# Performance work log

Measured on AMD Instinct MI355X. Metric: run time of the kernel, lower is better.

The kernel has to match this reference:

```python
import jax, jax.numpy as jnp
import numpy as np


def setup_inputs() -> dict:
    key = jax.random.key(0)
    X = jax.random.normal(key, (8, 64, 64, 64), dtype=jnp.float32)
    return {"X": X}


def reference(X):
    N, C, h, w = X.shape
    x1 = X.reshape(N, C, h * w)            # [N, C, HW]
    x2 = jnp.transpose(x1, (0, 2, 1))      # [N, HW, C]
    scores = jnp.einsum('bnc,bcm->bnm', x2, x1)  # [N, HW, HW]
    c = jax.nn.softmax(scores, axis=2)
    out = jnp.einsum('bnm,bmc->bnc', c, x2)      # [N, HW, C]
    out = jnp.transpose(out, (0, 2, 1)).reshape(N, C, h, w)
    return out
```

## Files before the change

kernel.cpp:

```cpp
#include <hip/hip_runtime.h>
#include <math.h>


#define SEQ 4096
#define DIM 64
#define LDB 72
#define LDO 68
#define LDS2 68
#define QSCALE 1.2011224087864498f

typedef __attribute__((ext_vector_type(8))) short  short8;
typedef __attribute__((ext_vector_type(4))) float  f32x4;

__device__ __forceinline__ unsigned short f2bf(float f) {
    union { float f; unsigned int u; } x; x.f = f;
    unsigned int u = x.u + 0x7FFFu + ((x.u >> 16) & 1u);
    return (unsigned short)(u >> 16);
}
__device__ __forceinline__ float bf2f(unsigned short h) {
    union { unsigned int u; float f; } x; x.u = ((unsigned int)h) << 16; return x.f;
}
__device__ __forceinline__ float fast_exp2(float x) {
#if __has_builtin(__builtin_amdgcn_exp2f)
    return __builtin_amdgcn_exp2f(x);
#else
    float r;
    asm("v_exp_f32 %0, %1\n\ts_nop 0" : "=v"(r) : "v"(x));
    return r;
#endif
}
__device__ __forceinline__ float fast_rcp(float x) {
#if __has_builtin(__builtin_amdgcn_rcpf)
    return __builtin_amdgcn_rcpf(x);
#else
    return 1.f / x;
#endif
}

__global__ __launch_bounds__(256) void prepass4(const float* __restrict__ X,
                                                unsigned short* __restrict__ Kf,
                                                unsigned short* __restrict__ Vf,
                                                float* __restrict__ Norms,
                                                float* __restrict__ MaxPart) {
    __shared__ __align__(16) unsigned short sT[64 * LDS2];
    __shared__ __align__(16) unsigned short sVu[64 * LDS2];
    __shared__ float sRed[4];
    const int b = blockIdx.y, m0 = blockIdx.x * 64;
    const float* Xb = X + (size_t)b * DIM * SEQ;
    const int t = threadIdx.x, w = t >> 6;
    const int mw = t & 15, cg = t >> 4;

    #pragma unroll
    for (int cr = 0; cr < 4; ++cr) {
        const int c = cg * 4 + cr;
        const f32x4 v = *(const f32x4*)(Xb + (size_t)c * SEQ + m0 + 4 * mw);
        *(ushort4*)(sVu + c * LDS2 + 4 * mw) =
            make_ushort4(f2bf(v.x), f2bf(v.y), f2bf(v.z), f2bf(v.w));
        sT[(4 * mw + 0) * LDS2 + c] = f2bf(v.x * QSCALE);
        sT[(4 * mw + 1) * LDS2 + c] = f2bf(v.y * QSCALE);
        sT[(4 * mw + 2) * LDS2 + c] = f2bf(v.z * QSCALE);
        sT[(4 * mw + 3) * LDS2 + c] = f2bf(v.w * QSCALE);
    }
    __syncthreads();
    const int m = t >> 2, ck = t & 3;

    const short8 a0 = *(const short8*)(sT + m * LDS2 + ck * 16);
    const short8 a1 = *(const short8*)(sT + m * LDS2 + ck * 16 + 8);
    {
        const size_t base = (size_t)b * 262144 + (size_t)(m0 >> 5) * 2048;
        #pragma unroll
        for (int j = 0; j < 2; ++j) {
            const int chunk = 2 * ck + j;
            const int tile = m >> 5, mt = (m >> 4) & 1;
            const int quad = chunk & 3, ks = chunk >> 2;
            const size_t off = base + (size_t)(tile * 4 + mt * 2 + ks) * 512
                                    + (size_t)(quad * 16 + (m & 15)) * 8;
            *(short8*)(Kf + off) = j ? a1 : a0;
        }
    }
    float s = 0.f;
    #pragma unroll
    for (int i = 0; i < 8; ++i) {
        const float f0 = bf2f((unsigned short)a0[i]);
        const float f1 = bf2f((unsigned short)a1[i]);
        s += f0 * f0 + f1 * f1;
    }
    s += __shfl_xor(s, 1);
    s += __shfl_xor(s, 2);
    const float nm = sqrtf(s);
    if (ck == 0) Norms[(size_t)b * SEQ + m0 + m] = nm;

    {
        const int ctv = (t >> 6) & 3, lv = t & 63;
        const int qv = lv >> 4, l15v = lv & 15;
        const int cidx = (16 * ctv + l15v) * LDS2;
        const size_t vbase = (size_t)b * 262144 + (size_t)(m0 >> 5) * 2048
                           + (size_t)ctv * 512 + (size_t)lv * 8;
        #pragma unroll
        for (int tl = 0; tl < 2; ++tl) {
            const ushort4 g0 = *(const ushort4*)(sVu + cidx + tl * 32 + 4 * qv);
            const ushort4 g1 = *(const ushort4*)(sVu + cidx + tl * 32 + 16 + 4 * qv);
            union { ushort4 g[2]; short8 v; } cat;
            cat.g[0] = g0; cat.g[1] = g1;
            *(short8*)(Vf + vbase + (size_t)tl * 2048) = cat.v;
        }
    }

    float mx = nm;
    #pragma unroll
    for (int d = 4; d < 64; d <<= 1) mx = fmaxf(mx, __shfl_xor(mx, d));
    if ((t & 63) == 0) sRed[w] = mx;
    __syncthreads();
    if (t == 0)
        MaxPart[b * 64 + blockIdx.x] =
            fmaxf(fmaxf(sRed[0], sRed[1]), fmaxf(sRed[2], sRed[3]));
}

#define LOADK(DST)                                                                 \
    {                                                                              \
        _Pragma("unroll")                                                          \
        for (int mt_ = 0; mt_ < 2; ++mt_) {                                        \
            _Pragma("unroll")                                                      \
            for (int ks_ = 0; ks_ < 2; ++ks_)                                      \
                DST[mt_][ks_] = *(const short8*)(kp + (mt_ * 2 + ks_) * 512);      \
        }                                                                          \
    }

#define LOADV(DST)                                                                 \
    {                                                                              \
        _Pragma("unroll")                                                          \
        for (int ct_ = 0; ct_ < 4; ++ct_)                                          \
            DST[ct_] = *(const short8*)(vp + ct_ * 512);                           \
    }

#define ATTN_STEP(KF, VF)                                                          \
    {                                                                              \
        f32x4 a_[2][2];                                                            \
        __builtin_amdgcn_s_setprio(1);                                             \
        _Pragma("unroll")                                                          \
        for (int qt_ = 0; qt_ < 2; ++qt_) {                                        \
            _Pragma("unroll")                                                      \
            for (int mt_ = 0; mt_ < 2; ++mt_) {                                    \
                f32x4 s_ = cin[qt_];                                               \
                s_ = __builtin_amdgcn_mfma_f32_16x16x32_bf16(KF[mt_][0], qf[qt_][0], s_, 0, 0, 0); \
                s_ = __builtin_amdgcn_mfma_f32_16x16x32_bf16(KF[mt_][1], qf[qt_][1], s_, 0, 0, 0); \
                a_[qt_][mt_] = s_;                                                 \
            }                                                                      \
        }                                                                          \
        __builtin_amdgcn_s_setprio(0);                                             \
        short8 pa_[2];                                                             \
        _Pragma("unroll")                                                          \
        for (int qt_ = 0; qt_ < 2; ++qt_) {                                        \
            union { unsigned u[4]; short8 v; } pk_;                                \
            _Pragma("unroll")                                                      \
            for (int mt_ = 0; mt_ < 2; ++mt_) {                                    \
                const float p0_ = fast_exp2(a_[qt_][mt_][0]);                      \
                const float p1_ = fast_exp2(a_[qt_][mt_][1]);                      \
                const float p2_ = fast_exp2(a_[qt_][mt_][2]);                      \
                const float p3_ = fast_exp2(a_[qt_][mt_][3]);                      \
                lp4[qt_] += (f32x4){p0_, p1_, p2_, p3_};                           \
                pk_.u[2 * mt_ + 0] = __builtin_amdgcn_perm(__float_as_uint(p1_), __float_as_uint(p0_), 0x07060302u); \
                pk_.u[2 * mt_ + 1] = __builtin_amdgcn_perm(__float_as_uint(p3_), __float_as_uint(p2_), 0x07060302u); \
            }                                                                      \
            pa_[qt_] = pk_.v;                                                      \
        }                                                                          \
        __builtin_amdgcn_s_setprio(1);                                             \
        _Pragma("unroll")                                                          \
        for (int qt_ = 0; qt_ < 2; ++qt_) {                                        \
            _Pragma("unroll")                                                      \
            for (int ct_ = 0; ct_ < 4; ++ct_)                                      \
                acc_o[qt_][ct_] = __builtin_amdgcn_mfma_f32_16x16x32_bf16(pa_[qt_], VF[ct_], acc_o[qt_][ct_], 0, 0, 0); \
        }                                                                          \
        __builtin_amdgcn_s_setprio(0);                                             \
    }

template <bool PARTIAL>
__global__ __launch_bounds__(128) void attn_split4(const unsigned short* __restrict__ Kf,
                                                   const unsigned short* __restrict__ Vf,
                                                   const float* __restrict__ Norms,
                                                   const float* __restrict__ MaxPart,
                                                   unsigned short* __restrict__ Obf,
                                                   float* __restrict__ Lbase,
                                                   float* __restrict__ Out,
                                                   int niter) {
    __shared__ __align__(16) float sO[64 * LDO];

    const int tid  = threadIdx.x;
    const int lane = tid & 63;
    const int w    = tid >> 6;
    const int l15  = lane & 15;
    const int quad = lane >> 4;

    const int b   = blockIdx.y;
    const int s0  = blockIdx.x * 64;
    const int h   = blockIdx.z;
    const int kt0 = h * niter;
    const unsigned short* Kfb = Kf + (size_t)b * 262144;
    const unsigned short* Vfb = Vf + (size_t)b * 262144;

    float mxn = MaxPart[b * 64 + lane];
    #pragma unroll
    for (int d = 1; d < 64; d <<= 1) mxn = fmaxf(mxn, __shfl_xor(mxn, d));

    short8 qf[2][2];
    f32x4 cin[2];
    const int qtile = (s0 + 32 * w) >> 5;
    #pragma unroll
    for (int qt = 0; qt < 2; ++qt) {
        #pragma unroll
        for (int ks = 0; ks < 2; ++ks)
            qf[qt][ks] = *(const short8*)(Kfb + (size_t)(qtile * 4 + qt * 2 + ks) * 512 + lane * 8);
        const float mrow = Norms[(size_t)b * SEQ + s0 + 32 * w + 16 * qt + l15] * mxn;
        cin[qt] = (f32x4){-mrow, -mrow, -mrow, -mrow};
    }

    f32x4 acc_o[2][4];
    #pragma unroll
    for (int qt = 0; qt < 2; ++qt)
        #pragma unroll
        for (int ct = 0; ct < 4; ++ct) acc_o[qt][ct] = (f32x4){0.f, 0.f, 0.f, 0.f};
    f32x4 lp4[2];
    lp4[0] = (f32x4){0.f, 0.f, 0.f, 0.f};
    lp4[1] = (f32x4){0.f, 0.f, 0.f, 0.f};

    const unsigned short* kp = Kfb + (size_t)kt0 * 2048 + lane * 8;
    const unsigned short* vp = Vfb + (size_t)kt0 * 2048 + lane * 8;

    short8 kA[2][2], kB[2][2];
    LOADK(kA);
    kp += 2048;

    for (int it = 0; it < niter; it += 2) {
        short8 vfA[4];
        LOADV(vfA); vp += 2048;
        LOADK(kB);  kp += 2048;
        ATTN_STEP(kA, vfA);

        short8 vfB[4];
        LOADV(vfB); vp += 2048;
        LOADK(kA);  kp += 2048;
        ATTN_STEP(kB, vfB);
    }

    float lp[2];
    #pragma unroll
    for (int qt = 0; qt < 2; ++qt) {
        lp[qt] = (lp4[qt][0] + lp4[qt][1]) + (lp4[qt][2] + lp4[qt][3]);
        lp[qt] += __shfl_xor(lp[qt], 16);
        lp[qt] += __shfl_xor(lp[qt], 32);
    }

    if (PARTIAL) {
        if (quad == 0) {
            #pragma unroll
            for (int qt = 0; qt < 2; ++qt)
                (Lbase + (size_t)h * 8 * SEQ)[(size_t)b * SEQ + s0 + 32 * w + 16 * qt + l15] = lp[qt];
        }
    } else {
        #pragma unroll
        for (int qt = 0; qt < 2; ++qt) {
            float inv[4];
            #pragma unroll
            for (int r = 0; r < 4; ++r) inv[r] = fast_rcp(__shfl(lp[qt], 4 * quad + r));
            #pragma unroll
            for (int ct = 0; ct < 4; ++ct)
                #pragma unroll
                for (int r = 0; r < 4; ++r) acc_o[qt][ct][r] *= inv[r];
        }
    }

    #pragma unroll
    for (int qt = 0; qt < 2; ++qt)
        #pragma unroll
        for (int ct = 0; ct < 4; ++ct) {
            const int c = 16 * ct + l15;
            #pragma unroll
            for (int r = 0; r < 4; ++r)
                sO[c * LDO + 32 * w + 16 * qt + 4 * quad + r] = acc_o[qt][ct][r];
        }
    __syncthreads();
    const int mw = tid & 15, cg = tid >> 4;
    if (PARTIAL) {
        unsigned short* Op = Obf + (size_t)h * 8 * DIM * SEQ;
        #pragma unroll
        for (int cc = 0; cc < 8; ++cc) {
            const int c = cg + 8 * cc;
            const f32x4 v = *(const f32x4*)(sO + c * LDO + 4 * mw);
            *(ushort4*)(Op + ((size_t)b * DIM + c) * SEQ + s0 + 4 * mw) =
                make_ushort4(f2bf(v.x), f2bf(v.y), f2bf(v.z), f2bf(v.w));
        }
    } else {
        #pragma unroll
        for (int cc = 0; cc < 8; ++cc) {
            const int c = cg + 8 * cc;
            const f32x4 v = *(const f32x4*)(sO + c * LDO + 4 * mw);
            *(f32x4*)(Out + ((size_t)b * DIM + c) * SEQ + s0 + 4 * mw) = v;
        }
    }
}

__global__ __launch_bounds__(256) void combine4(const unsigned short* __restrict__ Obf,
                                                const float* __restrict__ Lp,
                                                float* __restrict__ Out) {
    const int gid = blockIdx.x * 256 + threadIdx.x;
    const size_t base = (size_t)gid * 4;
    const int s = (int)(base & 4095);
    const int b = (int)(base >> 18);
    f32x4 os = (f32x4){0.f, 0.f, 0.f, 0.f};
    f32x4 ls = (f32x4){0.f, 0.f, 0.f, 0.f};
    #pragma unroll
    for (int h = 0; h < 4; ++h) {
        const ushort4 o = *(const ushort4*)(Obf + (size_t)h * 2097152 + base);
        os[0] += bf2f(o.x); os[1] += bf2f(o.y); os[2] += bf2f(o.z); os[3] += bf2f(o.w);
        const f32x4 l = *(const f32x4*)(Lp + (size_t)h * 8 * SEQ + b * SEQ + s);
        #pragma unroll
        for (int i = 0; i < 4; ++i) ls[i] += l[i];
    }
    f32x4 o;
    #pragma unroll
    for (int i = 0; i < 4; ++i) o[i] = os[i] / ls[i];
    *(f32x4*)(Out + base) = o;
}

__global__ __launch_bounds__(256, 2) void attn_fallback(const float* __restrict__ X,
                                                        float* __restrict__ Out) {
    __shared__ __align__(16) unsigned char smem[27648];
    unsigned short* sK = (unsigned short*)smem;
    unsigned short* sV = (unsigned short*)(smem + 9216);
    unsigned short* sP = (unsigned short*)(smem + 18432);
    float*          sO = (float*)smem;
    const int tid  = threadIdx.x;
    const int lane = tid & 63;
    const int w    = tid >> 6;
    const int l15  = lane & 15;
    const int quad = lane >> 4;
    const int b  = blockIdx.y;
    const int s0 = blockIdx.x * 64;
    const float* Xb = X + (size_t)b * DIM * SEQ;
    const int mgrp = tid & 15;
    const int c0   = tid >> 4;

    for (int cc = 0; cc < 4; ++cc) {
        int c = c0 + 16 * cc;
        const f32x4 v = *(const f32x4*)(Xb + (size_t)c * SEQ + s0 + 4 * mgrp);
        sK[(4 * mgrp + 0) * LDB + c] = f2bf(v.x);
        sK[(4 * mgrp + 1) * LDB + c] = f2bf(v.y);
        sK[(4 * mgrp + 2) * LDB + c] = f2bf(v.z);
        sK[(4 * mgrp + 3) * LDB + c] = f2bf(v.w);
    }
    __syncthreads();
    short8 qf0, qf1;
    {
        const int row = 16 * w + l15;
        qf0 = *(const short8*)(sK + row * LDB + quad * 8);
        qf1 = *(const short8*)(sK + row * LDB + 32 + quad * 8);
    }
    __syncthreads();
    f32x4 acc_o[4];
    for (int ct = 0; ct < 4; ++ct) acc_o[ct] = (f32x4){0.f, 0.f, 0.f, 0.f};
    float m_i[4] = {-1e30f, -1e30f, -1e30f, -1e30f};
    float l_i[4] = {0.f, 0.f, 0.f, 0.f};
    for (int kt = 0; kt < SEQ / 64; ++kt) {
        const int m0 = kt * 64;
        for (int cc = 0; cc < 4; ++cc) {
            int c = c0 + 16 * cc;
            const f32x4 v = *(const f32x4*)(Xb + (size_t)c * SEQ + m0 + 4 * mgrp);
            unsigned short h0 = f2bf(v.x), h1 = f2bf(v.y), h2 = f2bf(v.z), h3 = f2bf(v.w);
            *(ushort4*)(sV + c * LDB + 4 * mgrp) = make_ushort4(h0, h1, h2, h3);
            sK[(4 * mgrp + 0) * LDB + c] = h0;
            sK[(4 * mgrp + 1) * LDB + c] = h1;
            sK[(4 * mgrp + 2) * LDB + c] = h2;
            sK[(4 * mgrp + 3) * LDB + c] = h3;
        }
        __syncthreads();
        short8 vf[2][4];
        for (int ks = 0; ks < 2; ++ks)
            for (int ct = 0; ct < 4; ++ct)
                vf[ks][ct] = *(const short8*)(sV + (16 * ct + l15) * LDB + ks * 32 + quad * 8);
        f32x4 acc_s[4];
        for (int mt = 0; mt < 4; ++mt) {
            const int row = 16 * mt + l15;
            const short8 kf0 = *(const short8*)(sK + row * LDB + quad * 8);
            const short8 kf1 = *(const short8*)(sK + row * LDB + 32 + quad * 8);
            f32x4 a = (f32x4){0.f, 0.f, 0.f, 0.f};
            a = __builtin_amdgcn_mfma_f32_16x16x32_bf16(qf0, kf0, a, 0, 0, 0);
            a = __builtin_amdgcn_mfma_f32_16x16x32_bf16(qf1, kf1, a, 0, 0, 0);
            acc_s[mt] = a;
        }
        float alpha[4];
        for (int r = 0; r < 4; ++r) {
            float mx = fmaxf(fmaxf(acc_s[0][r], acc_s[1][r]), fmaxf(acc_s[2][r], acc_s[3][r]));
            mx = fmaxf(mx, __shfl_xor(mx, 1));
            mx = fmaxf(mx, __shfl_xor(mx, 2));
            mx = fmaxf(mx, __shfl_xor(mx, 4));
            mx = fmaxf(mx, __shfl_xor(mx, 8));
            const float mnew = fmaxf(m_i[r], mx);
            alpha[r] = __expf(m_i[r] - mnew);
            m_i[r] = mnew;
        }
        float rowsum[4] = {0.f, 0.f, 0.f, 0.f};
        unsigned short pb[4][4];
        for (int mt = 0; mt < 4; ++mt)
            for (int r = 0; r < 4; ++r) {
                const float p = __expf(acc_s[mt][r] - m_i[r]);
                rowsum[r] += p;
                pb[mt][r] = f2bf(p);
            }
        for (int r = 0; r < 4; ++r) {
            float s = rowsum[r];
            s += __shfl_xor(s, 1);
            s += __shfl_xor(s, 2);
            s += __shfl_xor(s, 4);
            s += __shfl_xor(s, 8);
            l_i[r] = alpha[r] * l_i[r] + s;
        }
        for (int ct = 0; ct < 4; ++ct)
            for (int r = 0; r < 4; ++r)
                acc_o[ct][r] *= alpha[r];
        for (int mt = 0; mt < 4; ++mt)
            for (int r = 0; r < 4; ++r)
                sP[(16 * w + quad * 4 + r) * LDB + l15 + 16 * mt] = pb[mt][r];
        __syncthreads();
        const short8 pf0 = *(const short8*)(sP + (16 * w + l15) * LDB + quad * 8);
        const short8 pf1 = *(const short8*)(sP + (16 * w + l15) * LDB + 32 + quad * 8);
        for (int ct = 0; ct < 4; ++ct) {
            acc_o[ct] = __builtin_amdgcn_mfma_f32_16x16x32_bf16(pf0, vf[0][ct], acc_o[ct], 0, 0, 0);
            acc_o[ct] = __builtin_amdgcn_mfma_f32_16x16x32_bf16(pf1, vf[1][ct], acc_o[ct], 0, 0, 0);
        }
    }
    float inv[4];
    for (int r = 0; r < 4; ++r) inv[r] = 1.f / l_i[r];
    for (int ct = 0; ct < 4; ++ct) {
        const int c = 16 * ct + l15;
        for (int r = 0; r < 4; ++r)
            sO[c * LDO + 16 * w + quad * 4 + r] = acc_o[ct][r] * inv[r];
    }
    __syncthreads();
    for (int cc = 0; cc < 4; ++cc) {
        const int c = c0 + 16 * cc;
        const f32x4 v = *(const f32x4*)(sO + c * LDO + 4 * mgrp);
        *(f32x4*)(Out + (size_t)b * DIM * SEQ + (size_t)c * SEQ + s0 + 4 * mgrp) = v;
    }
}

extern "C" void kernel_launch(void* const* d_in, const int* in_sizes, int n_in,
                              void* d_out, int out_size, void* d_ws, size_t ws_size,
                              hipStream_t stream) {
    const float* X = (const float*)d_in[0];
    float* Out = (float*)d_out;
    const size_t elems = (size_t)8 * SEQ * DIM;
    const size_t offVf    = elems * 2;
    const size_t offNorms = offVf + elems * 2;
    const size_t offMaxP  = offNorms + (size_t)8 * SEQ * 4;
    const size_t offObf   = offMaxP + 8 * 64 * 4;
    const size_t offLp    = offObf + 4 * elems * 2;
    const size_t need     = offLp + 4 * (size_t)8 * SEQ * 4;

    if (ws_size >= need) {
        unsigned short* Kf = (unsigned short*)d_ws;
        unsigned short* Vf = (unsigned short*)((char*)d_ws + offVf);
        float* Norms   = (float*)((char*)d_ws + offNorms);
        float* MaxPart = (float*)((char*)d_ws + offMaxP);
        unsigned short* Obf = (unsigned short*)((char*)d_ws + offObf);
        float* Lp = (float*)((char*)d_ws + offLp);
        prepass4<<<dim3(64, 8), 256, 0, stream>>>(X, Kf, Vf, Norms, MaxPart);
        attn_split4<true><<<dim3(64, 8, 4), 128, 0, stream>>>(Kf, Vf, Norms, MaxPart,
                                                              Obf, Lp, nullptr, 32);
        combine4<<<(int)(elems / 1024), 256, 0, stream>>>(Obf, Lp, Out);
    } else {
        attn_fallback<<<dim3(64, 8), 256, 0, stream>>>(X, Out);
    }
}
```

Before: 118.5 us.

## Double query rows per wave in split attention to reuse K/V fragments

Each wave now handles 64 query rows (four 16-row tiles) instead of 32. Every K/V fragment loaded from memory therefore feeds twice as many MFMAs, and the grid is halved to 32x8x4 blocks. Block indices are remapped so batch is the fastest-varying dimension, the s_setprio hints are dropped, and the LDS output staging uses a new odd row stride. The cost is higher register use (more accumulators and Q fragments), fewer blocks to fill the GPU, and 16-byte LDS reads on a stride of 133 floats that may not be 16-byte aligned.

```diff
diff --git a/kernel.cpp b/kernel.cpp
--- a/kernel.cpp
+++ b/kernel.cpp
@@ -6,6 +6,7 @@
 #define DIM 64
 #define LDB 72
 #define LDO 68
+#define LDO2 133
 #define LDS2 68
 #define QSCALE 1.2011224087864498f
 
@@ -135,10 +136,9 @@
 
 #define ATTN_STEP(KF, VF)                                                          \
     {                                                                              \
-        f32x4 a_[2][2];                                                            \
-        __builtin_amdgcn_s_setprio(1);                                             \
+        f32x4 a_[4][2];                                                            \
         _Pragma("unroll")                                                          \
-        for (int qt_ = 0; qt_ < 2; ++qt_) {                                        \
+        for (int qt_ = 0; qt_ < 4; ++qt_) {                                        \
             _Pragma("unroll")                                                      \
             for (int mt_ = 0; mt_ < 2; ++mt_) {                                    \
                 f32x4 s_ = cin[qt_];                                               \
@@ -147,10 +147,9 @@
                 a_[qt_][mt_] = s_;                                                 \
             }                                                                      \
         }                                                                          \
-        __builtin_amdgcn_s_setprio(0);                                             \
-        short8 pa_[2];                                                             \
+        short8 pa_[4];                                                             \
         _Pragma("unroll")                                                          \
-        for (int qt_ = 0; qt_ < 2; ++qt_) {                                        \
+        for (int qt_ = 0; qt_ < 4; ++qt_) {                                        \
             union { unsigned u[4]; short8 v; } pk_;                                \
             _Pragma("unroll")                                                      \
             for (int mt_ = 0; mt_ < 2; ++mt_) {                                    \
@@ -164,26 +163,24 @@
             }                                                                      \
             pa_[qt_] = pk_.v;                                                      \
         }                                                                          \
-        __builtin_amdgcn_s_setprio(1);                                             \
         _Pragma("unroll")                                                          \
-        for (int qt_ = 0; qt_ < 2; ++qt_) {                                        \
+        for (int qt_ = 0; qt_ < 4; ++qt_) {                                        \
             _Pragma("unroll")                                                      \
             for (int ct_ = 0; ct_ < 4; ++ct_)                                      \
                 acc_o[qt_][ct_] = __builtin_amdgcn_mfma_f32_16x16x32_bf16(pa_[qt_], VF[ct_], acc_o[qt_][ct_], 0, 0, 0); \
         }                                                                          \
-        __builtin_amdgcn_s_setprio(0);                                             \
     }
 
 template <bool PARTIAL>
-__global__ __launch_bounds__(128) void attn_split4(const unsigned short* __restrict__ Kf,
-                                                   const unsigned short* __restrict__ Vf,
-                                                   const float* __restrict__ Norms,
-                                                   const float* __restrict__ MaxPart,
-                                                   unsigned short* __restrict__ Obf,
-                                                   float* __restrict__ Lbase,
-                                                   float* __restrict__ Out,
-                                                   int niter) {
-    __shared__ __align__(16) float sO[64 * LDO];
+__global__ __launch_bounds__(128, 2) void attn_split4(const unsigned short* __restrict__ Kf,
+                                                      const unsigned short* __restrict__ Vf,
+                                                      const float* __restrict__ Norms,
+                                                      const float* __restrict__ MaxPart,
+                                                      unsigned short* __restrict__ Obf,
+                                                      float* __restrict__ Lbase,
+                                                      float* __restrict__ Out,
+                                                      int niter) {
+    __shared__ __align__(16) float sO[64 * LDO2];
 
     const int tid  = threadIdx.x;
     const int lane = tid & 63;
@@ -191,10 +188,12 @@
     const int l15  = lane & 15;
     const int quad = lane >> 4;
 
-    const int b   = blockIdx.y;
-    const int s0  = blockIdx.x * 64;
-    const int h   = blockIdx.z;
-    const int kt0 = h * niter;
+    const int gid  = blockIdx.x + 32 * (blockIdx.y + 8 * blockIdx.z);
+    const int b    = gid & 7;
+    const int rest = gid >> 3;
+    const int s0   = (rest & 31) * 128;
+    const int h    = rest >> 5;
+    const int kt0  = h * niter;
     const unsigned short* Kfb = Kf + (size_t)b * 262144;
     const unsigned short* Vfb = Vf + (size_t)b * 262144;
 
@@ -202,26 +201,27 @@
     #pragma unroll
     for (int d = 1; d < 64; d <<= 1) mxn = fmaxf(mxn, __shfl_xor(mxn, d));
 
-    short8 qf[2][2];
-    f32x4 cin[2];
-    const int qtile = (s0 + 32 * w) >> 5;
-    #pragma unroll
-    for (int qt = 0; qt < 2; ++qt) {
+    short8 qf[4][2];
+    f32x4 cin[4];
+    const int qtile = (s0 + 64 * w) >> 5;
+    #pragma unroll
+    for (int qt = 0; qt < 4; ++qt) {
         #pragma unroll
         for (int ks = 0; ks < 2; ++ks)
-            qf[qt][ks] = *(const short8*)(Kfb + (size_t)(qtile * 4 + qt * 2 + ks) * 512 + lane * 8);
-        const float mrow = Norms[(size_t)b * SEQ + s0 + 32 * w + 16 * qt + l15] * mxn;
+            qf[qt][ks] = *(const short8*)(Kfb
+                + (size_t)((qtile + (qt >> 1)) * 4 + (qt & 1) * 2 + ks) * 512 + lane * 8);
+        const float mrow = Norms[(size_t)b * SEQ + s0 + 64 * w + 16 * qt + l15] * mxn;
         cin[qt] = (f32x4){-mrow, -mrow, -mrow, -mrow};
     }
 
-    f32x4 acc_o[2][4];
-    #pragma unroll
-    for (int qt = 0; qt < 2; ++qt)
+    f32x4 acc_o[4][4];
+    #pragma unroll
+    for (int qt = 0; qt < 4; ++qt)
         #pragma unroll
         for (int ct = 0; ct < 4; ++ct) acc_o[qt][ct] = (f32x4){0.f, 0.f, 0.f, 0.f};
-    f32x4 lp4[2];
-    lp4[0] = (f32x4){0.f, 0.f, 0.f, 0.f};
-    lp4[1] = (f32x4){0.f, 0.f, 0.f, 0.f};
+    f32x4 lp4[4];
+    #pragma unroll
+    for (int qt = 0; qt < 4; ++qt) lp4[qt] = (f32x4){0.f, 0.f, 0.f, 0.f};
 
     const unsigned short* kp = Kfb + (size_t)kt0 * 2048 + lane * 8;
     const unsigned short* vp = Vfb + (size_t)kt0 * 2048 + lane * 8;
@@ -242,9 +242,9 @@
         ATTN_STEP(kB, vfB);
     }
 
-    float lp[2];
-    #pragma unroll
-    for (int qt = 0; qt < 2; ++qt) {
+    float lp[4];
+    #pragma unroll
+    for (int qt = 0; qt < 4; ++qt) {
         lp[qt] = (lp4[qt][0] + lp4[qt][1]) + (lp4[qt][2] + lp4[qt][3]);
         lp[qt] += __shfl_xor(lp[qt], 16);
         lp[qt] += __shfl_xor(lp[qt], 32);
@@ -253,12 +253,12 @@
     if (PARTIAL) {
         if (quad == 0) {
             #pragma unroll
-            for (int qt = 0; qt < 2; ++qt)
-                (Lbase + (size_t)h * 8 * SEQ)[(size_t)b * SEQ + s0 + 32 * w + 16 * qt + l15] = lp[qt];
+            for (int qt = 0; qt < 4; ++qt)
+                (Lbase + (size_t)h * 8 * SEQ)[(size_t)b * SEQ + s0 + 64 * w + 16 * qt + l15] = lp[qt];
         }
     } else {
         #pragma unroll
-        for (int qt = 0; qt < 2; ++qt) {
+        for (int qt = 0; qt < 4; ++qt) {
             float inv[4];
             #pragma unroll
             for (int r = 0; r < 4; ++r) inv[r] = fast_rcp(__shfl(lp[qt], 4 * quad + r));
@@ -270,30 +270,30 @@
     }
 
     #pragma unroll
-    for (int qt = 0; qt < 2; ++qt)
+    for (int qt = 0; qt < 4; ++qt)
         #pragma unroll
         for (int ct = 0; ct < 4; ++ct) {
             const int c = 16 * ct + l15;
             #pragma unroll
             for (int r = 0; r < 4; ++r)
-                sO[c * LDO + 32 * w + 16 * qt + 4 * quad + r] = acc_o[qt][ct][r];
-        }
-    __syncthreads();
-    const int mw = tid & 15, cg = tid >> 4;
+                sO[c * LDO2 + 64 * w + 16 * qt + 4 * quad + r] = acc_o[qt][ct][r];
+        }
+    __syncthreads();
+    const int mw = tid & 31, cg = tid >> 5;
     if (PARTIAL) {
         unsigned short* Op = Obf + (size_t)h * 8 * DIM * SEQ;
         #pragma unroll
-        for (int cc = 0; cc < 8; ++cc) {
-            const int c = cg + 8 * cc;
-            const f32x4 v = *(const f32x4*)(sO + c * LDO + 4 * mw);
+        for (int cc = 0; cc < 16; ++cc) {
+            const int c = cg + 4 * cc;
+            const f32x4 v = *(const f32x4*)(sO + c * LDO2 + 4 * mw);
             *(ushort4*)(Op + ((size_t)b * DIM + c) * SEQ + s0 + 4 * mw) =
                 make_ushort4(f2bf(v.x), f2bf(v.y), f2bf(v.z), f2bf(v.w));
         }
     } else {
         #pragma unroll
-        for (int cc = 0; cc < 8; ++cc) {
-            const int c = cg + 8 * cc;
-            const f32x4 v = *(const f32x4*)(sO + c * LDO + 4 * mw);
+        for (int cc = 0; cc < 16; ++cc) {
+            const int c = cg + 4 * cc;
+            const f32x4 v = *(const f32x4*)(sO + c * LDO2 + 4 * mw);
             *(f32x4*)(Out + ((size_t)b * DIM + c) * SEQ + s0 + 4 * mw) = v;
         }
     }
@@ -464,7 +464,7 @@
         unsigned short* Obf = (unsigned short*)((char*)d_ws + offObf);
         float* Lp = (float*)((char*)d_ws + offLp);
         prepass4<<<dim3(64, 8), 256, 0, stream>>>(X, Kf, Vf, Norms, MaxPart);
-        attn_split4<true><<<dim3(64, 8, 4), 128, 0, stream>>>(Kf, Vf, Norms, MaxPart,
+        attn_split4<true><<<dim3(32, 8, 4), 128, 0, stream>>>(Kf, Vf, Norms, MaxPart,
                                                               Obf, Lp, nullptr, 32);
         combine4<<<(int)(elems / 1024), 256, 0, stream>>>(Obf, Lp, Out);
     } else {
```

Measured after the change: 105.7 us. -10.8%, faster.
